# Kernel tuning notes

Measured on AMD Instinct MI355X. Metric: run time of the kernel, lower is better.

The kernel has to match this reference:

```python
import jax, jax.numpy as jnp
import numpy as np

WINDOW = 16
STRIDE = 8
PADDING = 0
EPS = 1e-6


def setup_inputs() -> dict:
    key = jax.random.key(0)
    x = jax.random.normal(key, (4, 32, 256, 256), dtype=jnp.float32)
    return {"x": x}


def reference(x):
    # Faithful translation of ExtractTensorPatches.forward:
    # grouped conv2d with an (identity + eps) one-hot kernel per channel,
    # so out_i = patch_elem_i + eps * sum(patch).
    B, C, H, W = x.shape
    w2 = WINDOW * WINDOW
    # (w2, 1, w, w): diag = 1+eps, off-diag = eps (matches create_kernel)
    k = (jnp.eye(w2, dtype=x.dtype) + jnp.asarray(EPS, x.dtype)).reshape(
        w2, 1, WINDOW, WINDOW
    )
    k = jnp.tile(k, (C, 1, 1, 1))  # (C*w2, 1, w, w), group-major like torch repeat
    out = jax.lax.conv_general_dilated(
        x,
        k,
        window_strides=(STRIDE, STRIDE),
        padding=[(PADDING, PADDING), (PADDING, PADDING)],
        feature_group_count=C,
        dimension_numbers=("NCHW", "OIHW", "NCHW"),
    )  # (B, C*w2, Ho, Wo)
    Ho, Wo = out.shape[2], out.shape[3]
    out = out.reshape(B, C, WINDOW, WINDOW, Ho * Wo)
    return jnp.transpose(out, (0, 4, 1, 2, 3))  # (B, L, C, w, w)
```

## Files before the change

kernel.cpp:

```cpp
#include <hip/hip_runtime.h>


#define BB   4
#define CC   32
#define HH   256
#define WW   256
#define WIN  16
#define STR  8
#define HO   31
#define WO   31
#define LL   (HO * WO)
#define EPSF 1e-6f

__global__ __launch_bounds__(256) void
extract_patches_kernel(const float* __restrict__ x, float* __restrict__ out) {
    const int lane = threadIdx.x & 63;
    const int wave = threadIdx.x >> 6;

    const int c  = (blockIdx.x << 2) + wave;
    const int l  = blockIdx.y;
    const int b  = blockIdx.z;
    const int ho = l / WO;
    const int wo = l - ho * WO;

    const int r  = lane >> 2;
    const int cq = lane & 3;

    const size_t in_off =
        (((size_t)(b * CC + c) * HH + (size_t)(ho * STR + r)) * WW) +
        (size_t)(wo * STR + cq * 4);
    const float4 v = *(const float4*)(x + in_off);

    float s = v.x + v.y + v.z + v.w;
#pragma unroll
    for (int off = 32; off; off >>= 1) s += __shfl_xor(s, off, 64);

    const float e = EPSF * s;
    const float4 o = make_float4(v.x + e, v.y + e, v.z + e, v.w + e);

    const size_t out_off =
        ((size_t)((b * LL + l) * CC + c) << 8) + (size_t)(lane << 2);
    *(float4*)(out + out_off) = o;
}

extern "C" void kernel_launch(void* const* d_in, const int* in_sizes, int n_in,
                              void* d_out, int out_size, void* d_ws, size_t ws_size,
                              hipStream_t stream) {
    const float* x = (const float*)d_in[0];
    float* out = (float*)d_out;

    dim3 grid(CC / 4, LL, BB);
    dim3 block(256);
    extract_patches_kernel<<<grid, block, 0, stream>>>(x, out);
}
```

Measured before the change: 160.9 us.

## Stage 16-row input strips in LDS and reuse across overlapping patches

Each block now loads a full 16x256 row strip of one channel into shared memory once. It computes 8x8 column-block sums there, combines them into per-patch epsilon sums, and then writes all 31 patches of that output row from LDS. This removes the roughly 4x redundant global reads of overlapping windows and the per-patch cross-lane reduction. The cost is two block barriers, LDS usage, and a smaller grid of larger blocks.

New measurement: 148.6 us. 7.6% less time.

```diff
diff --git a/kernel.cpp b/kernel.cpp
--- a/kernel.cpp
+++ b/kernel.cpp
@@ -5,42 +5,67 @@
 #define CC   32
 #define HH   256
 #define WW   256
-#define WIN  16
 #define STR  8
-#define HO   31
-#define WO   31
-#define LL   (HO * WO)
+#define HOC  31
+#define WOC  31
+#define LL   (HOC * WOC)
 #define EPSF 1e-6f
+#define PITCH 272
 
 __global__ __launch_bounds__(256) void
-extract_patches_kernel(const float* __restrict__ x, float* __restrict__ out) {
-    const int lane = threadIdx.x & 63;
-    const int wave = threadIdx.x >> 6;
+extract_patches_strip(const float* __restrict__ x, float* __restrict__ out) {
+    __shared__ float strip[16 * PITCH];
+    __shared__ float cs[16 * 32];
+    __shared__ float epsP[32];
 
-    const int c  = (blockIdx.x << 2) + wave;
-    const int l  = blockIdx.y;
-    const int b  = blockIdx.z;
-    const int ho = l / WO;
-    const int wo = l - ho * WO;
+    const int tid = threadIdx.x;
+    const int c   = blockIdx.x;
+    const int ho  = blockIdx.y;
+    const int b   = blockIdx.z;
 
-    const int r  = lane >> 2;
-    const int cq = lane & 3;
+    const float* src = x + ((size_t)(b * CC + c) * HH + (size_t)(ho * STR)) * WW;
 
-    const size_t in_off =
-        (((size_t)(b * CC + c) * HH + (size_t)(ho * STR + r)) * WW) +
-        (size_t)(wo * STR + cq * 4);
-    const float4 v = *(const float4*)(x + in_off);
+#pragma unroll
+    for (int it = 0; it < 4; ++it) {
+        const int g   = (it * 256 + tid) * 4;
+        const float4 v = *(const float4*)(src + g);
+        const int row = g >> 8;
+        const int col = g & 255;
+        *(float4*)(&strip[row * PITCH + col]) = v;
+        float s4 = v.x + v.y + v.z + v.w;
+        s4 += __shfl_xor(s4, 1, 64);
+        if ((tid & 1) == 0)
+            cs[g >> 3] = s4;
+    }
+    __syncthreads();
 
-    float s = v.x + v.y + v.z + v.w;
+    if (tid < WOC) {
+        float s = 0.f;
 #pragma unroll
-    for (int off = 32; off; off >>= 1) s += __shfl_xor(s, off, 64);
+        for (int r = 0; r < 16; ++r)
+            s += cs[r * 32 + 2 * tid] + cs[r * 32 + 2 * tid + 1];
+        epsP[tid] = EPSF * s;
+    }
+    __syncthreads();
 
-    const float e = EPSF * s;
-    const float4 o = make_float4(v.x + e, v.y + e, v.z + e, v.w + e);
-
-    const size_t out_off =
-        ((size_t)((b * LL + l) * CC + c) << 8) + (size_t)(lane << 2);
-    *(float4*)(out + out_off) = o;
+    const int wave  = tid >> 6;
+    const int lane  = tid & 63;
+    const int prow  = lane >> 2;
+    const int pcol4 = (lane & 3) * 4;
+    float* dstbase = out
+        + (((size_t)b * LL + (size_t)ho * WOC) * CC + c) * 256
+        + (size_t)(lane * 4);
+#pragma unroll
+    for (int p = 0; p < 8; ++p) {
+        const int wo = p * 4 + wave;
+        if (wo < WOC) {
+            const float4 v =
+                *(const float4*)(&strip[prow * PITCH + wo * STR + pcol4]);
+            const float e = epsP[wo];
+            const float4 o = make_float4(v.x + e, v.y + e, v.z + e, v.w + e);
+            *(float4*)(dstbase + ((size_t)wo << 13)) = o;
+        }
+    }
 }
 
 extern "C" void kernel_launch(void* const* d_in, const int* in_sizes, int n_in,
@@ -49,7 +74,7 @@
     const float* x = (const float*)d_in[0];
     float* out = (float*)d_out;
 
-    dim3 grid(CC / 4, LL, BB);
+    dim3 grid(CC, HOC, BB);
     dim3 block(256);
-    extract_patches_kernel<<<grid, block, 0, stream>>>(x, out);
+    extract_patches_strip<<<grid, block, 0, stream>>>(x, out);
 }
```
